# Kernel tuning notes

Measured on AMD Instinct MI355X. Metric: run time of the kernel, lower is better.

The kernel has to match this reference:

```python
import jax, jax.numpy as jnp
import numpy as np

INPUTSIZE = 1024
OUTPUTSIZE = 1024
FEATUREMAPS = 16
BITS = (INPUTSIZE - 1).bit_length()  # 10
BATCH = 2048


def _make_fm():
    # fm[k, j, i] = (i ^ (1 << j)) % inputsize  (same for every feature map k)
    i = np.arange(OUTPUTSIZE, dtype=np.int64)
    j = (1 << np.arange(BITS, dtype=np.int64))[:, None]
    fm_bits_out = (i[None, :] ^ j) % INPUTSIZE  # [bits, out]
    fm = np.broadcast_to(fm_bits_out[None], (FEATUREMAPS, BITS, OUTPUTSIZE)).copy()
    return jnp.asarray(fm, dtype=jnp.int32)


def setup_inputs() -> dict:
    key = jax.random.key(0)
    k1, k2, k3 = jax.random.split(key, 3)
    std = 0.5 / BITS
    x = jax.random.normal(k1, (BATCH, INPUTSIZE), dtype=jnp.float32)
    weights = jax.random.normal(k2, (FEATUREMAPS, BITS, OUTPUTSIZE), dtype=jnp.float32) * std
    bias = jax.random.normal(k3, (FEATUREMAPS, OUTPUTSIZE), dtype=jnp.float32) * std
    return {"x": x, "weights": weights, "bias": bias, "fm": _make_fm()}


def _resize(t, newsize):
    # Static-shape version of Layer.resize (column crop/tile)
    cur = t.shape[1]
    if newsize < cur:
        return t[:, :newsize]
    if newsize > cur:
        mult = (newsize + cur - 1) // cur
        return jnp.tile(t, (1, mult))[:, :newsize]
    return t


def reference(x, weights, bias, fm):
    # gather: [B, F, bits, O]
    gathered = x[:, fm]
    # multiply by weights [F, bits, O] and reduce over bits -> [B, F, O]
    net = jnp.einsum('bfjo,fjo->bfo', gathered, weights) + bias
    flat = net.reshape(x.shape[0], FEATUREMAPS * OUTPUTSIZE)
    tiled = jnp.tile(_resize(x, OUTPUTSIZE), (1, FEATUREMAPS))
    return flat + tiled
```

## Files before the change

kernel.cpp:

```cpp
#include <hip/hip_runtime.h>


#define BTILE 32

__global__ __launch_bounds__(256, 4) void hypercube_kernel(
    const float* __restrict__ x,
    const float* __restrict__ w,
    const float* __restrict__ bias,
    float* __restrict__ out)
{
    const int lane  = threadIdx.x & 63;
    const int wave  = threadIdx.x >> 6;
    const int chunk = blockIdx.x & 15;
    const int btile = blockIdx.x >> 4;
    const int b0    = btile * BTILE;
    const int f0    = wave * 4;
    const int obase = chunk * 64;
    const int o     = obase + lane;

    float wr[4][10], br[4];
    #pragma unroll
    for (int ff = 0; ff < 4; ++ff) {
        const int f = f0 + ff;
        #pragma unroll
        for (int j = 0; j < 10; ++j)
            wr[ff][j] = w[(f * 10 + j) * 1024 + o];
        br[ff] = bias[f * 1024 + o];
    }

    const int a64  = (chunk ^ 1) * 64 + lane;
    const int a128 = (chunk ^ 2) * 64 + lane;
    const int a256 = (chunk ^ 4) * 64 + lane;
    const int a512 = (chunk ^ 8) * 64 + lane;

    #pragma unroll 2
    for (int bi = 0; bi < BTILE; ++bi) {
        const int b = b0 + bi;
        const float* __restrict__ xb = x + (size_t)b * 1024;

        const float x0   = xb[o];
        const float x64  = xb[a64];
        const float x128 = xb[a128];
        const float x256 = xb[a256];
        const float x512 = xb[a512];

        const float s0 = __shfl_xor(x0, 1);
        const float s1 = __shfl_xor(x0, 2);
        const float s2 = __shfl_xor(x0, 4);
        const float s3 = __shfl_xor(x0, 8);
        const float s4 = __shfl_xor(x0, 16);
        const float s5 = __shfl_xor(x0, 32);

        float* __restrict__ ob = out + (size_t)b * (16 * 1024) + obase + lane;
        #pragma unroll
        for (int ff = 0; ff < 4; ++ff) {
            float acc = br[ff] + x0;
            acc = fmaf(s0,   wr[ff][0], acc);
            acc = fmaf(s1,   wr[ff][1], acc);
            acc = fmaf(s2,   wr[ff][2], acc);
            acc = fmaf(s3,   wr[ff][3], acc);
            acc = fmaf(s4,   wr[ff][4], acc);
            acc = fmaf(s5,   wr[ff][5], acc);
            acc = fmaf(x64,  wr[ff][6], acc);
            acc = fmaf(x128, wr[ff][7], acc);
            acc = fmaf(x256, wr[ff][8], acc);
            acc = fmaf(x512, wr[ff][9], acc);
            ob[(size_t)(f0 + ff) * 1024] = acc;
        }
    }
}

extern "C" void kernel_launch(void* const* d_in, const int* in_sizes, int n_in,
                              void* d_out, int out_size, void* d_ws, size_t ws_size,
                              hipStream_t stream) {
    const float* x    = (const float*)d_in[0];
    const float* w    = (const float*)d_in[1];
    const float* bias = (const float*)d_in[2];
    float* out = (float*)d_out;

    dim3 grid(16 * (2048 / BTILE));
    dim3 block(256);
    hypercube_kernel<<<grid, block, 0, stream>>>(x, w, bias, out);
}
```

Measured before the change: 159.3 us.

## Prefetch next x rows into registers, use nontemporal stores, halve batch tile

Software-pipelines the batch loop: the x values for the next two rows are loaded into registers while the current two rows are computed and stored. Output writes become nontemporal stores so the large output stream bypasses cache. BTILE drops from 32 to 16, doubling the grid and raising parallelism. Costs are extra registers, plus one redundant prefetch of rows 0 and 1 on the last iteration.

```diff
diff --git a/kernel.cpp b/kernel.cpp
--- a/kernel.cpp
+++ b/kernel.cpp
@@ -1,7 +1,7 @@
 #include <hip/hip_runtime.h>
 
 
-#define BTILE 32
+#define BTILE 16
 
 __global__ __launch_bounds__(256, 4) void hypercube_kernel(
     const float* __restrict__ x,
@@ -33,39 +33,68 @@
     const int a256 = (chunk ^ 4) * 64 + lane;
     const int a512 = (chunk ^ 8) * 64 + lane;
 
-    #pragma unroll 2
-    for (int bi = 0; bi < BTILE; ++bi) {
-        const int b = b0 + bi;
-        const float* __restrict__ xb = x + (size_t)b * 1024;
+    const float* __restrict__ xb = x + (size_t)b0 * 1024;
 
-        const float x0   = xb[o];
-        const float x64  = xb[a64];
-        const float x128 = xb[a128];
-        const float x256 = xb[a256];
-        const float x512 = xb[a512];
+    float cx0[2], cx64[2], cx128[2], cx256[2], cx512[2];
+    #pragma unroll
+    for (int r = 0; r < 2; ++r) {
+        const float* __restrict__ xr = xb + r * 1024;
+        cx0[r]   = xr[o];
+        cx64[r]  = xr[a64];
+        cx128[r] = xr[a128];
+        cx256[r] = xr[a256];
+        cx512[r] = xr[a512];
+    }
 
-        const float s0 = __shfl_xor(x0, 1);
-        const float s1 = __shfl_xor(x0, 2);
-        const float s2 = __shfl_xor(x0, 4);
-        const float s3 = __shfl_xor(x0, 8);
-        const float s4 = __shfl_xor(x0, 16);
-        const float s5 = __shfl_xor(x0, 32);
+    #pragma unroll 1
+    for (int bi = 0; bi < BTILE; bi += 2) {
+        const int pb = (bi + 2 < BTILE) ? (bi + 2) : 0;
+        float nx0[2], nx64[2], nx128[2], nx256[2], nx512[2];
+        #pragma unroll
+        for (int r = 0; r < 2; ++r) {
+            const float* __restrict__ xr = xb + (size_t)(pb + r) * 1024;
+            nx0[r]   = xr[o];
+            nx64[r]  = xr[a64];
+            nx128[r] = xr[a128];
+            nx256[r] = xr[a256];
+            nx512[r] = xr[a512];
+        }
 
-        float* __restrict__ ob = out + (size_t)b * (16 * 1024) + obase + lane;
         #pragma unroll
-        for (int ff = 0; ff < 4; ++ff) {
-            float acc = br[ff] + x0;
-            acc = fmaf(s0,   wr[ff][0], acc);
-            acc = fmaf(s1,   wr[ff][1], acc);
-            acc = fmaf(s2,   wr[ff][2], acc);
-            acc = fmaf(s3,   wr[ff][3], acc);
-            acc = fmaf(s4,   wr[ff][4], acc);
-            acc = fmaf(s5,   wr[ff][5], acc);
-            acc = fmaf(x64,  wr[ff][6], acc);
-            acc = fmaf(x128, wr[ff][7], acc);
-            acc = fmaf(x256, wr[ff][8], acc);
-            acc = fmaf(x512, wr[ff][9], acc);
-            ob[(size_t)(f0 + ff) * 1024] = acc;
+        for (int r = 0; r < 2; ++r) {
+            const int b = b0 + bi + r;
+            const float s0 = __shfl_xor(cx0[r], 1);
+            const float s1 = __shfl_xor(cx0[r], 2);
+            const float s2 = __shfl_xor(cx0[r], 4);
+            const float s3 = __shfl_xor(cx0[r], 8);
+            const float s4 = __shfl_xor(cx0[r], 16);
+            const float s5 = __shfl_xor(cx0[r], 32);
+
+            float* __restrict__ ob = out + (size_t)b * (16 * 1024) + obase + lane;
+            #pragma unroll
+            for (int ff = 0; ff < 4; ++ff) {
+                float acc = br[ff] + cx0[r];
+                acc = fmaf(s0,       wr[ff][0], acc);
+                acc = fmaf(s1,       wr[ff][1], acc);
+                acc = fmaf(s2,       wr[ff][2], acc);
+                acc = fmaf(s3,       wr[ff][3], acc);
+                acc = fmaf(s4,       wr[ff][4], acc);
+                acc = fmaf(s5,       wr[ff][5], acc);
+                acc = fmaf(cx64[r],  wr[ff][6], acc);
+                acc = fmaf(cx128[r], wr[ff][7], acc);
+                acc = fmaf(cx256[r], wr[ff][8], acc);
+                acc = fmaf(cx512[r], wr[ff][9], acc);
+                __builtin_nontemporal_store(acc, &ob[(size_t)(f0 + ff) * 1024]);
+            }
+        }
+
+        #pragma unroll
+        for (int r = 0; r < 2; ++r) {
+            cx0[r]   = nx0[r];
+            cx64[r]  = nx64[r];
+            cx128[r] = nx128[r];
+            cx256[r] = nx256[r];
+            cx512[r] = nx512[r];
         }
     }
 }
```

Result: slower. 165.5 us (+3.9%).

## Stage x neighbor chunks in shared memory and widen per-wave feature maps

Applied to the files above, without the earlier changes.

Each block now preloads, with float4 loads, the five 64-wide x chunks that a batch tile needs into LDS and reads the hypercube neighbors from there, replacing the per-row global loads and the wave shuffles. Blocks shrink to two waves, each handling 8 feature maps with 80 weights in registers, and the batch tile is halved to 16 rows. The aim is fewer redundant global x reads and shuffles. In exchange register pressure rises and occupancy drops, while the kernel stays bound by the large output write.

```diff
diff --git a/kernel.cpp b/kernel.cpp
--- a/kernel.cpp
+++ b/kernel.cpp
@@ -1,26 +1,41 @@
 #include <hip/hip_runtime.h>
 
 
-#define BTILE 32
+#define BTILE 16
+#define NSLOT 5
 
-__global__ __launch_bounds__(256, 4) void hypercube_kernel(
+__global__ __launch_bounds__(128, 2) void hypercube_kernel(
     const float* __restrict__ x,
     const float* __restrict__ w,
     const float* __restrict__ bias,
     float* __restrict__ out)
 {
-    const int lane  = threadIdx.x & 63;
-    const int wave  = threadIdx.x >> 6;
+    __shared__ float xs[BTILE * NSLOT * 64];
+
+    const int tid   = threadIdx.x;
+    const int lane  = tid & 63;
+    const int wave  = tid >> 6;
     const int chunk = blockIdx.x & 15;
     const int btile = blockIdx.x >> 4;
     const int b0    = btile * BTILE;
-    const int f0    = wave * 4;
-    const int obase = chunk * 64;
-    const int o     = obase + lane;
+    const int f0    = wave * 8;
+    const int o     = chunk * 64 + lane;
 
-    float wr[4][10], br[4];
     #pragma unroll
-    for (int ff = 0; ff < 4; ++ff) {
+    for (int it = 0; it < (BTILE * NSLOT * 64 / 4) / 128; ++it) {
+        const int q    = it * 128 + tid;
+        const int row  = q / (NSLOT * 16);
+        const int rem  = q - row * (NSLOT * 16);
+        const int slot = rem >> 4;
+        const int l4   = (rem & 15) << 2;
+        const int src_chunk = chunk ^ ((1 << slot) >> 1);
+        const float4 v = *(const float4*)&x[(size_t)(b0 + row) * 1024 + src_chunk * 64 + l4];
+        *(float4*)&xs[q * 4] = v;
+    }
+
+    float wr[8][10], br[8];
+    #pragma unroll
+    for (int ff = 0; ff < 8; ++ff) {
         const int f = f0 + ff;
         #pragma unroll
         for (int j = 0; j < 10; ++j)
@@ -28,44 +43,38 @@
         br[ff] = bias[f * 1024 + o];
     }
 
-    const int a64  = (chunk ^ 1) * 64 + lane;
-    const int a128 = (chunk ^ 2) * 64 + lane;
-    const int a256 = (chunk ^ 4) * 64 + lane;
-    const int a512 = (chunk ^ 8) * 64 + lane;
+    __syncthreads();
 
     #pragma unroll 2
-    for (int bi = 0; bi < BTILE; ++bi) {
-        const int b = b0 + bi;
-        const float* __restrict__ xb = x + (size_t)b * 1024;
+    for (int row = 0; row < BTILE; ++row) {
+        const float* __restrict__ xr = &xs[row * (NSLOT * 64)];
+        const float x0 = xr[lane];
+        const float g0 = xr[lane ^ 1];
+        const float g1 = xr[lane ^ 2];
+        const float g2 = xr[lane ^ 4];
+        const float g3 = xr[lane ^ 8];
+        const float g4 = xr[lane ^ 16];
+        const float g5 = xr[lane ^ 32];
+        const float g6 = xr[64  + lane];
+        const float g7 = xr[128 + lane];
+        const float g8 = xr[192 + lane];
+        const float g9 = xr[256 + lane];
 
-        const float x0   = xb[o];
-        const float x64  = xb[a64];
-        const float x128 = xb[a128];
-        const float x256 = xb[a256];
-        const float x512 = xb[a512];
-
-        const float s0 = __shfl_xor(x0, 1);
-        const float s1 = __shfl_xor(x0, 2);
-        const float s2 = __shfl_xor(x0, 4);
-        const float s3 = __shfl_xor(x0, 8);
-        const float s4 = __shfl_xor(x0, 16);
-        const float s5 = __shfl_xor(x0, 32);
-
-        float* __restrict__ ob = out + (size_t)b * (16 * 1024) + obase + lane;
+        float* __restrict__ ob = out + (size_t)(b0 + row) * 16384 + chunk * 64 + lane;
         #pragma unroll
-        for (int ff = 0; ff < 4; ++ff) {
+        for (int ff = 0; ff < 8; ++ff) {
             float acc = br[ff] + x0;
-            acc = fmaf(s0,   wr[ff][0], acc);
-            acc = fmaf(s1,   wr[ff][1], acc);
-            acc = fmaf(s2,   wr[ff][2], acc);
-            acc = fmaf(s3,   wr[ff][3], acc);
-            acc = fmaf(s4,   wr[ff][4], acc);
-            acc = fmaf(s5,   wr[ff][5], acc);
-            acc = fmaf(x64,  wr[ff][6], acc);
-            acc = fmaf(x128, wr[ff][7], acc);
-            acc = fmaf(x256, wr[ff][8], acc);
-            acc = fmaf(x512, wr[ff][9], acc);
-            ob[(size_t)(f0 + ff) * 1024] = acc;
+            acc = fmaf(g0, wr[ff][0], acc);
+            acc = fmaf(g1, wr[ff][1], acc);
+            acc = fmaf(g2, wr[ff][2], acc);
+            acc = fmaf(g3, wr[ff][3], acc);
+            acc = fmaf(g4, wr[ff][4], acc);
+            acc = fmaf(g5, wr[ff][5], acc);
+            acc = fmaf(g6, wr[ff][6], acc);
+            acc = fmaf(g7, wr[ff][7], acc);
+            acc = fmaf(g8, wr[ff][8], acc);
+            acc = fmaf(g9, wr[ff][9], acc);
+            ob[(f0 + ff) * 1024] = acc;
         }
     }
 }
@@ -79,6 +88,6 @@
     float* out = (float*)d_out;
 
     dim3 grid(16 * (2048 / BTILE));
-    dim3 block(256);
+    dim3 block(128);
     hypercube_kernel<<<grid, block, 0, stream>>>(x, w, bias, out);
 }
```

Result: faster. 149.9 us (-5.9%).
